# Kernel tuning notes

Hardware: AMD Instinct MI355X
Metric: run time of the kernel (lower is better)

Reference implementation:

```python
import jax, jax.numpy as jnp
import numpy as np

B, T, I, H, C = 128, 1024, 256, 512, 10


def setup_inputs() -> dict:
    key = jax.random.key(0)
    ks = jax.random.split(key, 11)
    s1 = 1.0 / np.sqrt(H)
    u = lambda k, shp, s: jax.random.uniform(k, shp, jnp.float32, -s, s)
    return {
        "x": jax.random.normal(ks[0], (B, T, I), jnp.float32),
        "w_ih1": u(ks[1], (H, I), s1),
        "w_hh1": u(ks[2], (H, H), s1),
        "b_ih1": u(ks[3], (H,), s1),
        "b_hh1": u(ks[4], (H,), s1),
        "w_ih2": u(ks[5], (H, H), s1),
        "w_hh2": u(ks[6], (H, H), s1),
        "b_ih2": u(ks[7], (H,), s1),
        "b_hh2": u(ks[8], (H,), s1),
        "w_out": u(ks[9], (C, H), s1),
        "b_out": u(ks[10], (C,), s1),
    }


def reference(x, w_ih1, w_hh1, b_ih1, b_hh1, w_ih2, w_hh2, b_ih2, b_hh2, w_out, b_out):
    batch = x.shape[0]
    h0 = jnp.zeros((batch, H), x.dtype)

    def step(carry, x_t):
        h1, h2 = carry
        # cell 1: tanh(x_t @ w_ih1^T + b_ih1 + h1 @ w_hh1^T + b_hh1)
        h1 = jnp.tanh(x_t @ w_ih1.T + b_ih1 + h1 @ w_hh1.T + b_hh1)
        # cell 2 takes h1 as input
        h2 = jnp.tanh(h1 @ w_ih2.T + b_ih2 + h2 @ w_hh2.T + b_hh2)
        return (h1, h2), None

    # scan over time: x transposed to [T, B, I]
    (h1_T, h2_T), _ = jax.lax.scan(step, (h0, h0), jnp.swapaxes(x, 0, 1))
    return h2_T @ w_out.T + b_out
```

## Files before the change

kernel.cpp:

```cpp
#include <hip/hip_runtime.h>
#include <hip/hip_fp16.h>

#define Tt 1024
#define Ii 256
#define Hh 512
#define Cc 10
#define SPINMAX (1 << 20)

typedef _Float16 f16;
typedef _Float16 f16x8 __attribute__((ext_vector_type(8)));
typedef _Float16 f16x4 __attribute__((ext_vector_type(4)));
typedef _Float16 f16x2 __attribute__((ext_vector_type(2)));
typedef float    f32x4 __attribute__((ext_vector_type(4)));

#define OFF_WH1   32768u
#define OFF_WH2   557056u
#define OFF_XWR   1081344u
#define OFF_H1R   3178496u
#define OFF_PAR   5275648u

#define FLG(i) (FL + (size_t)(i) * 32)

static __device__ __forceinline__ f32x4 mfma16(f16x8 a, f16x8 b, f32x4 c) {
  return __builtin_amdgcn_mfma_f32_16x16x32_f16(a, b, c, 0, 0, 0);
}
static __device__ __forceinline__ float fast_tanh(float v) {
  float e = __expf(2.0f * v);
  return 1.0f - 2.0f / (e + 1.0f);
}
static __device__ __forceinline__ int ldflag(const int* p) {
  return __hip_atomic_load(p, __ATOMIC_RELAXED, __HIP_MEMORY_SCOPE_AGENT);
}
static __device__ __forceinline__ void stflag(int* p, int v) {
  __hip_atomic_store(p, v, __ATOMIC_RELAXED, __HIP_MEMORY_SCOPE_AGENT);
}
static __device__ __forceinline__ f16x4 ld64cc(const f16* p) {
  union { unsigned long long u; f16x4 v; } U;
  U.u = __hip_atomic_load((const unsigned long long*)p, __ATOMIC_RELAXED, __HIP_MEMORY_SCOPE_AGENT);
  return U.v;
}
static __device__ __forceinline__ void st64cc(f16* p, f16x4 v) {
  union { unsigned long long u; f16x4 v; } U; U.v = v;
  __hip_atomic_store((unsigned long long*)p, U.u, __ATOMIC_RELAXED, __HIP_MEMORY_SCOPE_AGENT);
}
static __device__ __forceinline__ f16x8 ld128cc(const f16* p) {
  union { unsigned long long u[2]; f16x8 v; } U;
  U.u[0] = __hip_atomic_load((const unsigned long long*)p,     __ATOMIC_RELAXED, __HIP_MEMORY_SCOPE_AGENT);
  U.u[1] = __hip_atomic_load((const unsigned long long*)p + 1, __ATOMIC_RELAXED, __HIP_MEMORY_SCOPE_AGENT);
  return U.v;
}
static __device__ __forceinline__ void stu32cc(unsigned* p, unsigned v) {
  __hip_atomic_store(p, v, __ATOMIC_RELAXED, __HIP_MEMORY_SCOPE_AGENT);
}
static __device__ __forceinline__ int imin(int a, int b) { return a < b ? a : b; }

#define VMFENCE() asm volatile("s_waitcnt vmcnt(0)" ::: "memory")
#define LBAR() do { asm volatile("s_waitcnt lgkmcnt(0)" ::: "memory"); \
                    __builtin_amdgcn_s_barrier(); \
                    __builtin_amdgcn_sched_barrier(0); } while (0)

__global__ void prep_weights(const float* __restrict__ w_hh1,
                             const float* __restrict__ w_hh2,
                             char* __restrict__ ws) {
  f16* wh1 = (f16*)(ws + OFF_WH1);
  f16* wh2 = (f16*)(ws + OFF_WH2);
  int i = blockIdx.x * 512 + threadIdx.x;
  if (i < 512 * 512) { wh1[i] = (f16)w_hh1[i]; wh2[i] = (f16)w_hh2[i]; }
}

#define BODY(P, FVC, HAVC)                                                        \
  if (!dead) {                                                                    \
    const int p_ = (P);                                                           \
    const int s0_ = p_ & 3;                                                       \
                \
    if (isH1 && p_ >= 16) {                                                       \
      int g_ = imin(imin(rGa, rGb), imin(rGc, rGd));                              \
      if (g_ < p_ - 15) {                                                         \
        const int* g0 = FLG(80 + bg * 16 + s0_ * 4);                              \
        int v_ = 0, sp_ = 0;                                                      \
        do { v_ = imin(imin(ldflag(g0), ldflag(g0 + 32)),                         \
                       imin(ldflag(g0 + 64), ldflag(g0 + 96)));                   \
             if (v_ >= p_ - 15) break; __builtin_amdgcn_s_sleep(2);               \
        } while (++sp_ < SPINMAX);                                                \
        if (v_ < p_ - 15) dead = 1;                                               \
      }                                                                           \
    }                                                                             \
                                            \
    if (!(HAVC) && !dead) {                                                       \
      int v_ = 0, sp_ = 0;                                                        \
      if (isH1) {                                                                 \
        const int* f0 = FLG(16 + bg * 8 + s0_ * 2);                               \
        do { v_ = imin(ldflag(f0), ldflag(f0 + 32)); if (v_ >= p_ + 1) break;     \
             __builtin_amdgcn_s_sleep(2); } while (++sp_ < SPINMAX);              \
      } else {                                                                    \
        const int* f0 = FLG(80 + bg * 16 + s0_ * 4);                              \
        do { v_ = imin(imin(ldflag(f0), ldflag(f0 + 32)),                         \
                       imin(ldflag(f0 + 64), ldflag(f0 + 96)));                   \
             if (v_ >= p_ + 1) break; __builtin_amdgcn_s_sleep(2);                \
        } while (++sp_ < SPINMAX);                                                \
      }                                                                           \
      if (v_ < p_ + 1) dead = 1;                                                  \
      const f16* fs_ = fring + ((size_t)(p_ & 15) * 8 + bg) * 8192;               \
      FVC[0] = ld64cc(fs_ + (wid * 4 + 0) * 256 + lm * 16 + lgrp * 4);            \
      FVC[1] = ld64cc(fs_ + (wid * 4 + 1) * 256 + lm * 16 + lgrp * 4);            \
      FVC[2] = ld64cc(fs_ + (wid * 4 + 2) * 256 + lm * 16 + lgrp * 4);            \
      FVC[3] = ld64cc(fs_ + (wid * 4 + 3) * 256 + lm * 16 + lgrp * 4);            \
    }                                                                             \
      \
    f16x8 w15_[4];                                                                \
    if (p_ > 0) {                                                                 \
      _Pragma("unroll")                                                           \
      for (int nt = 0; nt < 4; ++nt)                                              \
        w15_[nt] = *(const f16x8*)&whh[(size_t)(wcol0 + nt * 16 + lm) * 512 + 15 * 32 + lk8]; \
    }                                                                             \
    f32x4 acc[4];                                                                 \
    acc[0] = f32x4{0.f, 0.f, 0.f, 0.f};                                           \
    acc[1] = acc[0]; acc[2] = acc[0]; acc[3] = acc[0];                            \
    if (p_ > 0) {                                                                 \
      _Pragma("unroll")                                                           \
      for (int kc = 0; kc < 16; ++kc) {                                           \
        f16x8 A_ = *(const f16x8*)&sH[lm * 520 + kc * 32 + lk8];                  \
        _Pragma("unroll")                                                         \
        for (int nt = 0; nt < 4; ++nt) {                                          \
          f16x8 B_;                                                               \
          if (kc < 4)       B_ = *(const f16x8*)&sB[((size_t)(kc * 4 + lgrp) * 512 + wcol0 + nt * 16 + lm) * 8]; \
          else if (kc < 15) B_ = wbr[kc - 4][nt];                                 \
          else              B_ = w15_[nt];                                        \
          acc[nt] = mfma16(A_, B_, acc[nt]);                                      \
        }                                                                         \
      }                                                                           \
    }                                                                             \
    LBAR();                                                 \
        \
    if (p_ > 0) {                                                                 \
      if (isH1) {                                                                 \
        if ((p_ & 3) == 0) { VMFENCE(); if (tid == 0) stflag(progF, p_); }        \
      } else {                                                                    \
        if ((p_ & 1) == 0 && tid == 0) stflag(progF, p_);                         \
      }                                                                           \
    }                                                                             \
                                                                    \
    _Pragma("unroll")                                                             \
    for (int nt = 0; nt < 4; ++nt) {                                              \
      acc[nt][0] += (float)FVC[nt][0]; acc[nt][1] += (float)FVC[nt][1];           \
      acc[nt][2] += (float)FVC[nt][2]; acc[nt][3] += (float)FVC[nt][3];           \
    }                                                                             \
                   \
    HAVC = 0;                                                                     \
    if (p_ + 2 < Tt && !dead) {                                                   \
      int ca_ = isH1 ? imin(rFa, rFb) : imin(imin(rFa, rFb), imin(rFc, rFd));     \
      if (ca_ >= p_ + 3) {                                                        \
        const f16* fs_ = fring + ((size_t)((p_ + 2) & 15) * 8 + bg) * 8192;       \
        FVC[0] = ld64cc(fs_ + (wid * 4 + 0) * 256 + lm * 16 + lgrp * 4);          \
        FVC[1] = ld64cc(fs_ + (wid * 4 + 1) * 256 + lm * 16 + lgrp * 4);          \
        FVC[2] = ld64cc(fs_ + (wid * 4 + 2) * 256 + lm * 16 + lgrp * 4);          \
        FVC[3] = ld64cc(fs_ + (wid * 4 + 3) * 256 + lm * 16 + lgrp * 4);          \
        HAVC = 1;                                                                 \
      }                                                                           \
    }                                                                             \
                              \
    unsigned* ring32_ = (unsigned*)(h1r + ((size_t)(p_ & 15) * 8 + bg) * 8192);   \
    _Pragma("unroll")                                                             \
    for (int nt = 0; nt < 4; ++nt) {                                              \
      const int cp_ = (wcol0 + nt * 16 + lm) >> 1;                                \
      float v0_ = fast_tanh(acc[nt][0]), v1_ = fast_tanh(acc[nt][1]);             \
      float v2_ = fast_tanh(acc[nt][2]), v3_ = fast_tanh(acc[nt][3]);             \
      float o0_ = __shfl_xor(v0_, 1, 64), o1_ = __shfl_xor(v1_, 1, 64);           \
      float o2_ = __shfl_xor(v2_, 1, 64), o3_ = __shfl_xor(v3_, 1, 64);           \
      float m_[4] = {v0_, v1_, v2_, v3_}, q_[4] = {o0_, o1_, o2_, o3_};           \
      _Pragma("unroll")                                                           \
      for (int r2 = 0; r2 < 2; ++r2) {                                            \
        const int rr_ = rlo + r2, row_ = lgrp * 4 + rr_;                          \
        float ve_ = (lane & 1) ? q_[rr_] : m_[rr_];                               \
        float vo_ = (lane & 1) ? m_[rr_] : q_[rr_];                               \
        union { f16x2 h; unsigned u; } P_; P_.h = f16x2{(f16)ve_, (f16)vo_};      \
        sH32[row_ * 260 + cp_] = P_.u;                                            \
        if (isH1) stu32cc(ring32_ + row_ * 256 + cp_, P_.u);                      \
      }                                                                           \
    }                                                                             \
                  \
    if (isH1) {                                                                   \
      const int* f0 = FLG(16 + bg * 8 + (((p_ + 3) & 3)) * 2);                    \
      rFa = ldflag(f0); rFb = ldflag(f0 + 32);                                    \
      const int* g0 = FLG(80 + bg * 16 + (((p_ + 1) & 3)) * 4);                   \
      rGa = ldflag(g0); rGb = ldflag(g0 + 32);                                    \
      rGc = ldflag(g0 + 64); rGd = ldflag(g0 + 96);                               \
    } else {                                                                      \
      const int* f0 = FLG(80 + bg * 16 + (((p_ + 3) & 3)) * 4);                   \
      rFa = ldflag(f0); rFb = ldflag(f0 + 32);                                    \
      rFc = ldflag(f0 + 64); rFd = ldflag(f0 + 96);                               \
    }                                                                             \
    LBAR();                                             \
  }

__global__ __launch_bounds__(512) __attribute__((amdgpu_waves_per_eu(2, 2)))
void rnn_main(
    const float* __restrict__ x,
    const float* __restrict__ w_ih1, const float* __restrict__ w_ih2,
    const float* __restrict__ b_ih1, const float* __restrict__ b_hh1,
    const float* __restrict__ b_ih2, const float* __restrict__ b_hh2,
    const float* __restrict__ w_out, const float* __restrict__ b_out,
    float* __restrict__ out, char* __restrict__ ws)
{
  __shared__ __align__(16) char LS[147712];

  int* FL = (int*)ws;
  const f16* wh1f = (const f16*)(ws + OFF_WH1);
  const f16* wh2f = (const f16*)(ws + OFF_WH2);
  f16* xwr  = (f16*)(ws + OFF_XWR);
  f16* h1r  = (f16*)(ws + OFF_H1R);
  f16* parr = (f16*)(ws + OFF_PAR);

  const int bid  = blockIdx.x;
  const int tid  = threadIdx.x;
  const int wid  = tid >> 6;
  const int lane = tid & 63;
  const int lm   = lane & 15;
  const int lgrp = lane >> 4;
  const int lk8  = lgrp * 8;
  const int rlo  = (lane & 1) * 2;

  if (bid < 16) {
    const bool isH1 = (bid < 8);
    const int bg = bid & 7;
    f16* sB = (f16*)LS;
    f16* sH = (f16*)(LS + 131072);
    unsigned* sH32 = (unsigned*)sH;
    const f16* whh = isH1 ? wh1f : wh2f;
    const f16* fring = isH1 ? xwr : parr;
    int* progF = FLG(isH1 ? bg : 8 + bg);
    const int wcol0 = wid * 64;

    for (int i = tid; i < 8192; i += 512) {
      const int kc = i >> 11, grp = (i >> 9) & 3, col = i & 511;
      *(f16x8*)&sB[(size_t)i * 8] =
        *(const f16x8*)&whh[(size_t)col * 512 + kc * 32 + grp * 8];
    }
    for (int i = tid; i < 16 * 260; i += 512) sH32[i] = 0u;
    f16x8 wbr[11][4];
    #pragma unroll
    for (int kr = 0; kr < 11; ++kr) {
      #pragma unroll
      for (int nt = 0; nt < 4; ++nt) {
        wbr[kr][nt] = *(const f16x8*)&whh[(size_t)(wcol0 + nt * 16 + lm) * 512 + (kr + 4) * 32 + lk8];
        asm volatile("" : "+v"(wbr[kr][nt]));
      }
    }
    __syncthreads();

    int dead = 0;
    f16x4 fX[4], fY[4];
    int hX = 0, hY = 0;
    int rFa = 0, rFb = 0, rFc = 0, rFd = 0;
    int rGa = 0, rGb = 0, rGc = 0, rGd = 0;

    {
      int v = 0, sp = 0;
      if (isH1) {
        const int* f0 = FLG(16 + bg * 8 + 0);
        do { v = imin(ldflag(f0), ldflag(f0 + 32)); if (v >= 1) break;
             __builtin_amdgcn_s_sleep(8); } while (++sp < SPINMAX);
      } else {
        const int* f0 = FLG(80 + bg * 16 + 0);
        do { v = imin(imin(ldflag(f0), ldflag(f0 + 32)),
                      imin(ldflag(f0 + 64), ldflag(f0 + 96)));
             if (v >= 1) break; __builtin_amdgcn_s_sleep(8); } while (++sp < SPINMAX);
      }
      if (v < 1) dead = 1;
      const f16* fs = fring + (size_t)bg * 8192;
      #pragma unroll
      for (int nt = 0; nt < 4; ++nt)
        fX[nt] = ld64cc(fs + (wid * 4 + nt) * 256 + lm * 16 + lgrp * 4);
      hX = 1;
      v = 0; sp = 0;
      if (isH1) {
        const int* f0 = FLG(16 + bg * 8 + 1 * 2);
        do { v = imin(ldflag(f0), ldflag(f0 + 32)); if (v >= 2) break;
             __builtin_amdgcn_s_sleep(8); } while (++sp < SPINMAX);
      } else {
        const int* f0 = FLG(80 + bg * 16 + 1 * 4);
        do { v = imin(imin(ldflag(f0), ldflag(f0 + 32)),
                      imin(ldflag(f0 + 64), ldflag(f0 + 96)));
             if (v >= 2) break; __builtin_amdgcn_s_sleep(8); } while (++sp < SPINMAX);
      }
      if (v < 2) dead = 1;
      const f16* fs1 = fring + ((size_t)1 * 8 + bg) * 8192;
      #pragma unroll
      for (int nt = 0; nt < 4; ++nt)
        fY[nt] = ld64cc(fs1 + (wid * 4 + nt) * 256 + lm * 16 + lgrp * 4);
      hY = 1;
      if (isH1) {
        const int* a0 = FLG(16 + bg * 8 + 2 * 2);
        rFa = ldflag(a0); rFb = ldflag(a0 + 32);
      } else {
        const int* a0 = FLG(80 + bg * 16 + 2 * 4);
        rFa = ldflag(a0); rFb = ldflag(a0 + 32);
        rFc = ldflag(a0 + 64); rFd = ldflag(a0 + 96);
      }
    }

    for (int p2 = 0; p2 < Tt; p2 += 2) {
      BODY(p2,     fX, hX)
      BODY(p2 + 1, fY, hY)
    }

    VMFENCE();
    if (tid == 0) stflag(progF, Tt + 2);

    if (!isH1) {
      const int rl = wid * 2 + (lane >> 5);
      const int l32 = lane & 31;
      const f16* hr = &sH[rl * 520 + l32 * 16];
      f16x8 h0 = *(const f16x8*)hr;
      f16x8 h1v = *(const f16x8*)(hr + 8);
      float hf[16];
      #pragma unroll
      for (int j = 0; j < 8; ++j) { hf[j] = (float)h0[j]; hf[8 + j] = (float)h1v[j]; }
      #pragma unroll
      for (int c = 0; c < Cc; ++c) {
        const float* wr_ = w_out + (size_t)c * Hh + l32 * 16;
        float s = 0.f;
        #pragma unroll
        for (int j4 = 0; j4 < 4; ++j4) {
          float4 w4 = *(const float4*)(wr_ + j4 * 4);
          s += hf[j4*4]*w4.x + hf[j4*4+1]*w4.y + hf[j4*4+2]*w4.z + hf[j4*4+3]*w4.w;
        }
        #pragma unroll
        for (int off = 16; off >= 1; off >>= 1) s += __shfl_xor(s, off, 64);
        if (l32 == 0) out[(bg * 16 + rl) * Cc + c] = s + b_out[c];
      }
    }
  } else if (bid < 144) {
    const int idx = bid - 16;
    const int bg = idx >> 4, r16 = idx & 15;
    const int set = r16 >> 2, cb = r16 & 3;
    f16* sW = (f16*)LS;
    f16* sA = (f16*)(LS + 131072);

    for (int i = tid; i < 8192; i += 512) {
      const int kc = i >> 9, grp = (i >> 7) & 3, cl = i & 127;
      const float* sp = w_ih2 + (size_t)(cb * 128 + cl) * 512 + kc * 32 + grp * 8;
      float4 a = *(const float4*)sp, b = *(const float4*)(sp + 4);
      *(f16x8*)&sW[(size_t)i * 8] =
        f16x8{(f16)a.x,(f16)a.y,(f16)a.z,(f16)a.w,(f16)b.x,(f16)b.y,(f16)b.z,(f16)b.w};
    }
    const int gcol = cb * 128 + wid * 16 + lm;
    const float bias2v = b_ih2[gcol] + b_hh2[gcol];
    __syncthreads();

    int* myf = FLG(80 + bg * 16 + set * 4 + cb);
    const int* fH1 = FLG(bg);
    const int* fH2 = FLG(8 + bg);
    const int row_ = tid >> 5, c32 = tid & 31;
    int dead = 0;
    f16x8 R0, R1;
    {
      int v = 0, sp = 0;
      do { v = ldflag(fH1); if (v >= set + 1) break;
           __builtin_amdgcn_s_sleep(8); } while (++sp < SPINMAX);
      if (v < set + 1) dead = 1;
      const f16* hs = h1r + ((size_t)(set & 15) * 8 + bg) * 8192;
      R0 = ld128cc(hs + (size_t)tid * 16);
      R1 = ld128cc(hs + (size_t)tid * 16 + 8);
    }
    int rH1 = ldflag(fH1), rH2 = ldflag(fH2);

    for (int q = set; q < Tt && !dead; q += 4) {
      VMFENCE();
      *(f16x8*)&sA[row_ * 520 + c32 * 16]     = R0;
      *(f16x8*)&sA[row_ * 520 + c32 * 16 + 8] = R1;
      __syncthreads();
      f32x4 acc = {bias2v, bias2v, bias2v, bias2v};
      #pragma unroll
      for (int kc = 0; kc < 16; ++kc) {
        f16x8 A = *(const f16x8*)&sA[lm * 520 + kc * 32 + lk8];
        f16x8 B = *(const f16x8*)&sW[((size_t)(kc * 4 + lgrp) * 128 + wid * 16 + lm) * 8];
        acc = mfma16(A, B, acc);
      }
      st64cc(parr + ((size_t)(q & 15) * 8 + bg) * 8192 + (cb * 8 + wid) * 256 + lm * 16 + lgrp * 4,
             f16x4{(f16)acc[0], (f16)acc[1], (f16)acc[2], (f16)acc[3]});
      VMFENCE();
      if (tid == 0) stflag(myf, q + 1);
      const int nq = q + 4;
      if (nq < Tt) {
        int haveR = 0;
        if (rH1 >= nq + 1) {
          const f16* hs = h1r + ((size_t)(nq & 15) * 8 + bg) * 8192;
          R0 = ld128cc(hs + (size_t)tid * 16);
          R1 = ld128cc(hs + (size_t)tid * 16 + 8);
          haveR = 1;
        }
        if (nq >= 16 && rH2 < nq - 15) {
          int v = 0, sp = 0;
          do { v = ldflag(fH2); if (v >= nq - 15) break;
               __builtin_amdgcn_s_sleep(4); } while (++sp < SPINMAX);
          if (v < nq - 15) dead = 1;
        }
        if (!haveR && !dead) {
          int v = 0, sp = 0;
          do { v = ldflag(fH1); if (v >= nq + 1) break;
               __builtin_amdgcn_s_sleep(4); } while (++sp < SPINMAX);
          if (v < nq + 1) dead = 1;
          const f16* hs = h1r + ((size_t)(nq & 15) * 8 + bg) * 8192;
          R0 = ld128cc(hs + (size_t)tid * 16);
          R1 = ld128cc(hs + (size_t)tid * 16 + 8);
        }
      }
      rH1 = ldflag(fH1); rH2 = ldflag(fH2);
      __syncthreads();
    }
    VMFENCE();
    if (tid == 0) stflag(myf, Tt + 2);
  } else {
    const int idx = bid - 144;
    const int bg = idx >> 3, r8 = idx & 7;
    const int set = r8 >> 1, half = r8 & 1;
    f16* sW = (f16*)LS;

    for (int i = tid; i < 8192; i += 512) {
      const int kc = i >> 10, grp = (i >> 8) & 3, cl = i & 255;
      const float* sp = w_ih1 + (size_t)(half * 256 + cl) * 256 + kc * 32 + grp * 8;
      float4 a = *(const float4*)sp, b = *(const float4*)(sp + 4);
      *(f16x8*)&sW[(size_t)i * 8] =
        f16x8{(f16)a.x,(f16)a.y,(f16)a.z,(f16)a.w,(f16)b.x,(f16)b.y,(f16)b.z,(f16)b.w};
    }
    const int gc0 = half * 256 + wid * 32 + lm;
    const float b1v0 = b_ih1[gc0] + b_hh1[gc0];
    const float b1v1 = b_ih1[gc0 + 16] + b_hh1[gc0 + 16];
    __syncthreads();

    int* myf = FLG(16 + bg * 8 + set * 2 + half);
    const int* fH1 = FLG(bg);
    int rH1 = 0, dead = 0;
    for (int t = set; t < Tt && !dead; t += 4) {
      if (t >= 16 && rH1 < t - 15) {
        int v = 0, sp = 0;
        do { v = ldflag(fH1); if (v >= t - 15) break;
             __builtin_amdgcn_s_sleep(4); } while (++sp < SPINMAX);
        if (v < t - 15) dead = 1;
      }
      f32x4 acc0 = {b1v0, b1v0, b1v0, b1v0};
      f32x4 acc1 = {b1v1, b1v1, b1v1, b1v1};
      const float* xr = x + ((size_t)(bg * 16 + lm) * Tt + t) * Ii + lk8;
      #pragma unroll
      for (int kc = 0; kc < 8; ++kc) {
        float4 a = *(const float4*)(xr + kc * 32);
        float4 b = *(const float4*)(xr + kc * 32 + 4);
        f16x8 A{(f16)a.x,(f16)a.y,(f16)a.z,(f16)a.w,(f16)b.x,(f16)b.y,(f16)b.z,(f16)b.w};
        acc0 = mfma16(A, *(const f16x8*)&sW[((size_t)(kc*4+lgrp)*256 + wid*32 + lm)*8], acc0);
        acc1 = mfma16(A, *(const f16x8*)&sW[((size_t)(kc*4+lgrp)*256 + wid*32 + 16 + lm)*8], acc1);
      }
      f16* dst = xwr + ((size_t)(t & 15) * 8 + bg) * 8192;
      st64cc(dst + (half*16 + wid*2 + 0)*256 + lm*16 + lgrp*4,
             f16x4{(f16)acc0[0],(f16)acc0[1],(f16)acc0[2],(f16)acc0[3]});
      st64cc(dst + (half*16 + wid*2 + 1)*256 + lm*16 + lgrp*4,
             f16x4{(f16)acc1[0],(f16)acc1[1],(f16)acc1[2],(f16)acc1[3]});
      VMFENCE();
      if (tid == 0) stflag(myf, t + 1);
      rH1 = ldflag(fH1);
    }
    if (tid == 0) stflag(myf, Tt + 2);
  }
}

extern "C" void kernel_launch(void* const* d_in, const int* in_sizes, int n_in,
                              void* d_out, int out_size, void* d_ws, size_t ws_size,
                              hipStream_t stream) {
  (void)in_sizes; (void)n_in; (void)out_size; (void)ws_size;
  const float* x     = (const float*)d_in[0];
  const float* w_ih1 = (const float*)d_in[1];
  const float* w_hh1 = (const float*)d_in[2];
  const float* b_ih1 = (const float*)d_in[3];
  const float* b_hh1 = (const float*)d_in[4];
  const float* w_ih2 = (const float*)d_in[5];
  const float* w_hh2 = (const float*)d_in[6];
  const float* b_ih2 = (const float*)d_in[7];
  const float* b_hh2 = (const float*)d_in[8];
  const float* w_out = (const float*)d_in[9];
  const float* b_out = (const float*)d_in[10];
  float* out = (float*)d_out;
  char* ws = (char*)d_ws;

  hipMemsetAsync(ws, 0, 32768, stream);
  hipLaunchKernelGGL(prep_weights, dim3(512), dim3(512), 0, stream, w_hh1, w_hh2, ws);
  hipLaunchKernelGGL(rnn_main, dim3(208), dim3(512), 0, stream,
                     x, w_ih1, w_ih2, b_ih1, b_hh1, b_ih2, b_hh2,
                     w_out, b_out, out, ws);
}
```

Measured before the change: 8.190 ms.

## Halve block size to 256 threads, doubling per-wave output tiles

Every role of the persistent RNN kernel now runs with 4 waves per block instead of 8. Each wave computes twice as many 16-column MFMA tiles, holding more weight fragments in registers (a 10x8 register-resident block plus two streamed k-chunks). The aim is to cut block-wide barrier cost on the serial recurrence and reuse each A fragment across more MFMAs. The cost is much higher register pressure and fewer waves to hide latency, so spilling or exposed memory latency is possible.

```diff
diff --git a/kernel.cpp b/kernel.cpp
--- a/kernel.cpp
+++ b/kernel.cpp
@@ -68,11 +68,18 @@
   if (i < 512 * 512) { wh1[i] = (f16)w_hh1[i]; wh2[i] = (f16)w_hh2[i]; }
 }
 
+#define FEEDLOAD(DST, SLOT) {                                                     \
+    const f16* fs_ = fring + ((size_t)(SLOT) * 8 + bg) * 8192;                    \
+    _Pragma("unroll")                                                             \
+    for (int nt = 0; nt < 8; ++nt)                                                \
+      DST[nt] = ld64cc(fs_ + (wid * 8 + nt) * 256 + lm * 16 + lgrp * 4);          \
+  }
+
 #define BODY(P, FVC, HAVC)                                                        \
   if (!dead) {                                                                    \
     const int p_ = (P);                                                           \
     const int s0_ = p_ & 3;                                                       \
-                \
+               \
     if (isH1 && p_ >= 16) {                                                       \
       int g_ = imin(imin(rGa, rGb), imin(rGc, rGd));                              \
       if (g_ < p_ - 15) {                                                         \
@@ -100,38 +107,36 @@
         } while (++sp_ < SPINMAX);                                                \
       }                                                                           \
       if (v_ < p_ + 1) dead = 1;                                                  \
-      const f16* fs_ = fring + ((size_t)(p_ & 15) * 8 + bg) * 8192;               \
-      FVC[0] = ld64cc(fs_ + (wid * 4 + 0) * 256 + lm * 16 + lgrp * 4);            \
-      FVC[1] = ld64cc(fs_ + (wid * 4 + 1) * 256 + lm * 16 + lgrp * 4);            \
-      FVC[2] = ld64cc(fs_ + (wid * 4 + 2) * 256 + lm * 16 + lgrp * 4);            \
-      FVC[3] = ld64cc(fs_ + (wid * 4 + 3) * 256 + lm * 16 + lgrp * 4);            \
-    }                                                                             \
-      \
-    f16x8 w15_[4];                                                                \
+      FEEDLOAD(FVC, p_ & 15)                                                      \
+    }                                                                             \
+          \
+    f16x8 w14_[8], w15_[8];                                                       \
     if (p_ > 0) {                                                                 \
       _Pragma("unroll")                                                           \
-      for (int nt = 0; nt < 4; ++nt)                                              \
+      for (int nt = 0; nt < 8; ++nt) {                                            \
+        w14_[nt] = *(const f16x8*)&whh[(size_t)(wcol0 + nt * 16 + lm) * 512 + 14 * 32 + lk8]; \
         w15_[nt] = *(const f16x8*)&whh[(size_t)(wcol0 + nt * 16 + lm) * 512 + 15 * 32 + lk8]; \
-    }                                                                             \
-    f32x4 acc[4];                                                                 \
-    acc[0] = f32x4{0.f, 0.f, 0.f, 0.f};                                           \
-    acc[1] = acc[0]; acc[2] = acc[0]; acc[3] = acc[0];                            \
+      }                                                                           \
+    }                                                                             \
+    f32x4 acc[8];                                                                 \
+    _Pragma("unroll")                                                             \
+    for (int nt = 0; nt < 8; ++nt) acc[nt] = f32x4{0.f, 0.f, 0.f, 0.f};           \
     if (p_ > 0) {                                                                 \
       _Pragma("unroll")                                                           \
       for (int kc = 0; kc < 16; ++kc) {                                           \
         f16x8 A_ = *(const f16x8*)&sH[lm * 520 + kc * 32 + lk8];                  \
         _Pragma("unroll")                                                         \
-        for (int nt = 0; nt < 4; ++nt) {                                          \
+        for (int nt = 0; nt < 8; ++nt) {                                          \
           f16x8 B_;                                                               \
           if (kc < 4)       B_ = *(const f16x8*)&sB[((size_t)(kc * 4 + lgrp) * 512 + wcol0 + nt * 16 + lm) * 8]; \
-          else if (kc < 15) B_ = wbr[kc - 4][nt];                                 \
+          else if (kc < 14) B_ = wbr[kc - 4][nt];                                 \
+          else if (kc == 14) B_ = w14_[nt];                                       \
           else              B_ = w15_[nt];                                        \
           acc[nt] = mfma16(A_, B_, acc[nt]);                                      \
         }                                                                         \
       }                                                                           \
     }                                                                             \
-    LBAR();                                                 \
-        \
+    LBAR();                            \
     if (p_ > 0) {                                                                 \
       if (isH1) {                                                                 \
         if ((p_ & 3) == 0) { VMFENCE(); if (tid == 0) stflag(progF, p_); }        \
@@ -139,29 +144,21 @@
         if ((p_ & 1) == 0 && tid == 0) stflag(progF, p_);                         \
       }                                                                           \
     }                                                                             \
-                                                                    \
     _Pragma("unroll")                                                             \
-    for (int nt = 0; nt < 4; ++nt) {                                              \
+    for (int nt = 0; nt < 8; ++nt) {                                              \
       acc[nt][0] += (float)FVC[nt][0]; acc[nt][1] += (float)FVC[nt][1];           \
       acc[nt][2] += (float)FVC[nt][2]; acc[nt][3] += (float)FVC[nt][3];           \
     }                                                                             \
-                   \
+              \
     HAVC = 0;                                                                     \
     if (p_ + 2 < Tt && !dead) {                                                   \
       int ca_ = isH1 ? imin(rFa, rFb) : imin(imin(rFa, rFb), imin(rFc, rFd));     \
-      if (ca_ >= p_ + 3) {                                                        \
-        const f16* fs_ = fring + ((size_t)((p_ + 2) & 15) * 8 + bg) * 8192;       \
-        FVC[0] = ld64cc(fs_ + (wid * 4 + 0) * 256 + lm * 16 + lgrp * 4);          \
-        FVC[1] = ld64cc(fs_ + (wid * 4 + 1) * 256 + lm * 16 + lgrp * 4);          \
-        FVC[2] = ld64cc(fs_ + (wid * 4 + 2) * 256 + lm * 16 + lgrp * 4);          \
-        FVC[3] = ld64cc(fs_ + (wid * 4 + 3) * 256 + lm * 16 + lgrp * 4);          \
-        HAVC = 1;                                                                 \
-      }                                                                           \
+      if (ca_ >= p_ + 3) { FEEDLOAD(FVC, (p_ + 2) & 15) HAVC = 1; }               \
     }                                                                             \
                               \
     unsigned* ring32_ = (unsigned*)(h1r + ((size_t)(p_ & 15) * 8 + bg) * 8192);   \
     _Pragma("unroll")                                                             \
-    for (int nt = 0; nt < 4; ++nt) {                                              \
+    for (int nt = 0; nt < 8; ++nt) {                                              \
       const int cp_ = (wcol0 + nt * 16 + lm) >> 1;                                \
       float v0_ = fast_tanh(acc[nt][0]), v1_ = fast_tanh(acc[nt][1]);             \
       float v2_ = fast_tanh(acc[nt][2]), v3_ = fast_tanh(acc[nt][3]);             \
@@ -178,7 +175,7 @@
         if (isH1) stu32cc(ring32_ + row_ * 256 + cp_, P_.u);                      \
       }                                                                           \
     }                                                                             \
-                  \
+             \
     if (isH1) {                                                                   \
       const int* f0 = FLG(16 + bg * 8 + (((p_ + 3) & 3)) * 2);                    \
       rFa = ldflag(f0); rFb = ldflag(f0 + 32);                                    \
@@ -193,7 +190,7 @@
     LBAR();                                             \
   }
 
-__global__ __launch_bounds__(512) __attribute__((amdgpu_waves_per_eu(2, 2)))
+__global__ __launch_bounds__(256) __attribute__((amdgpu_waves_per_eu(1)))
 void rnn_main(
     const float* __restrict__ x,
     const float* __restrict__ w_ih1, const float* __restrict__ w_ih2,
@@ -229,19 +226,19 @@
     const f16* whh = isH1 ? wh1f : wh2f;
     const f16* fring = isH1 ? xwr : parr;
     int* progF = FLG(isH1 ? bg : 8 + bg);
-    const int wcol0 = wid * 64;
-
-    for (int i = tid; i < 8192; i += 512) {
+    const int wcol0 = wid * 128;
+
+    for (int i = tid; i < 8192; i += 256) {
       const int kc = i >> 11, grp = (i >> 9) & 3, col = i & 511;
       *(f16x8*)&sB[(size_t)i * 8] =
         *(const f16x8*)&whh[(size_t)col * 512 + kc * 32 + grp * 8];
     }
-    for (int i = tid; i < 16 * 260; i += 512) sH32[i] = 0u;
-    f16x8 wbr[11][4];
+    for (int i = tid; i < 16 * 260; i += 256) sH32[i] = 0u;
+    f16x8 wbr[10][8];
     #pragma unroll
-    for (int kr = 0; kr < 11; ++kr) {
-      #pragma unroll
-      for (int nt = 0; nt < 4; ++nt) {
+    for (int kr = 0; kr < 10; ++kr) {
+      #pragma unroll
+      for (int nt = 0; nt < 8; ++nt) {
         wbr[kr][nt] = *(const f16x8*)&whh[(size_t)(wcol0 + nt * 16 + lm) * 512 + (kr + 4) * 32 + lk8];
         asm volatile("" : "+v"(wbr[kr][nt]));
       }
@@ -249,7 +246,7 @@
     __syncthreads();
 
     int dead = 0;
-    f16x4 fX[4], fY[4];
+    f16x4 fX[8], fY[8];
     int hX = 0, hY = 0;
     int rFa = 0, rFb = 0, rFc = 0, rFd = 0;
     int rGa = 0, rGb = 0, rGc = 0, rGd = 0;
@@ -267,10 +264,7 @@
              if (v >= 1) break; __builtin_amdgcn_s_sleep(8); } while (++sp < SPINMAX);
       }
       if (v < 1) dead = 1;
-      const f16* fs = fring + (size_t)bg * 8192;
-      #pragma unroll
-      for (int nt = 0; nt < 4; ++nt)
-        fX[nt] = ld64cc(fs + (wid * 4 + nt) * 256 + lm * 16 + lgrp * 4);
+      FEEDLOAD(fX, 0)
       hX = 1;
       v = 0; sp = 0;
       if (isH1) {
@@ -284,10 +278,7 @@
              if (v >= 2) break; __builtin_amdgcn_s_sleep(8); } while (++sp < SPINMAX);
       }
       if (v < 2) dead = 1;
-      const f16* fs1 = fring + ((size_t)1 * 8 + bg) * 8192;
-      #pragma unroll
-      for (int nt = 0; nt < 4; ++nt)
-        fY[nt] = ld64cc(fs1 + (wid * 4 + nt) * 256 + lm * 16 + lgrp * 4);
+      FEEDLOAD(fY, 1)
       hY = 1;
       if (isH1) {
         const int* a0 = FLG(16 + bg * 8 + 2 * 2);
@@ -308,26 +299,31 @@
     if (tid == 0) stflag(progF, Tt + 2);
 
     if (!isH1) {
-      const int rl = wid * 2 + (lane >> 5);
-      const int l32 = lane & 31;
-      const f16* hr = &sH[rl * 520 + l32 * 16];
-      f16x8 h0 = *(const f16x8*)hr;
-      f16x8 h1v = *(const f16x8*)(hr + 8);
-      float hf[16];
-      #pragma unroll
-      for (int j = 0; j < 8; ++j) { hf[j] = (float)h0[j]; hf[8 + j] = (float)h1v[j]; }
+      const int rl  = wid * 4 + (lane >> 4);
+      const int l16 = lane & 15;
+      const f16* hr = &sH[rl * 520 + l16 * 32];
+      f16x8 a0 = *(const f16x8*)hr;
+      f16x8 a1 = *(const f16x8*)(hr + 8);
+      f16x8 a2 = *(const f16x8*)(hr + 16);
+      f16x8 a3 = *(const f16x8*)(hr + 24);
+      float hf[32];
+      #pragma unroll
+      for (int j = 0; j < 8; ++j) {
+        hf[j] = (float)a0[j]; hf[8 + j] = (float)a1[j];
+        hf[16 + j] = (float)a2[j]; hf[24 + j] = (float)a3[j];
+      }
       #pragma unroll
       for (int c = 0; c < Cc; ++c) {
-        const float* wr_ = w_out + (size_t)c * Hh + l32 * 16;
+        const float* wr_ = w_out + (size_t)c * Hh + l16 * 32;
         float s = 0.f;
         #pragma unroll
-        for (int j4 = 0; j4 < 4; ++j4) {
+        for (int j4 = 0; j4 < 8; ++j4) {
           float4 w4 = *(const float4*)(wr_ + j4 * 4);
           s += hf[j4*4]*w4.x + hf[j4*4+1]*w4.y + hf[j4*4+2]*w4.z + hf[j4*4+3]*w4.w;
         }
         #pragma unroll
-        for (int off = 16; off >= 1; off >>= 1) s += __shfl_xor(s, off, 64);
-        if (l32 == 0) out[(bg * 16 + rl) * Cc + c] = s + b_out[c];
+        for (int off = 8; off >= 1; off >>= 1) s += __shfl_xor(s, off, 64);
+        if (l16 == 0) out[(bg * 16 + rl) * Cc + c] = s + b_out[c];
       }
     }
   } else if (bid < 144) {
@@ -337,57 +333,63 @@
     f16* sW = (f16*)LS;
     f16* sA = (f16*)(LS + 131072);
 
-    for (int i = tid; i < 8192; i += 512) {
+    for (int i = tid; i < 8192; i += 256) {
       const int kc = i >> 9, grp = (i >> 7) & 3, cl = i & 127;
       const float* sp = w_ih2 + (size_t)(cb * 128 + cl) * 512 + kc * 32 + grp * 8;
       float4 a = *(const float4*)sp, b = *(const float4*)(sp + 4);
       *(f16x8*)&sW[(size_t)i * 8] =
         f16x8{(f16)a.x,(f16)a.y,(f16)a.z,(f16)a.w,(f16)b.x,(f16)b.y,(f16)b.z,(f16)b.w};
     }
-    const int gcol = cb * 128 + wid * 16 + lm;
-    const float bias2v = b_ih2[gcol] + b_hh2[gcol];
+    const int gcol = cb * 128 + wid * 32 + lm;
+    const float b2v0 = b_ih2[gcol] + b_hh2[gcol];
+    const float b2v1 = b_ih2[gcol + 16] + b_hh2[gcol + 16];
     __syncthreads();
 
     int* myf = FLG(80 + bg * 16 + set * 4 + cb);
     const int* fH1 = FLG(bg);
     const int* fH2 = FLG(8 + bg);
-    const int row_ = tid >> 5, c32 = tid & 31;
+    const int srow = tid >> 4;
+    const int soff = (tid & 15) * 32;
     int dead = 0;
-    f16x8 R0, R1;
+    f16x8 R0, R1, R2, R3;
     {
       int v = 0, sp = 0;
       do { v = ldflag(fH1); if (v >= set + 1) break;
            __builtin_amdgcn_s_sleep(8); } while (++sp < SPINMAX);
       if (v < set + 1) dead = 1;
-      const f16* hs = h1r + ((size_t)(set & 15) * 8 + bg) * 8192;
-      R0 = ld128cc(hs + (size_t)tid * 16);
-      R1 = ld128cc(hs + (size_t)tid * 16 + 8);
+      const f16* hs = h1r + ((size_t)(set & 15) * 8 + bg) * 8192 + (size_t)tid * 32;
+      R0 = ld128cc(hs); R1 = ld128cc(hs + 8); R2 = ld128cc(hs + 16); R3 = ld128cc(hs + 24);
     }
     int rH1 = ldflag(fH1), rH2 = ldflag(fH2);
 
     for (int q = set; q < Tt && !dead; q += 4) {
       VMFENCE();
-      *(f16x8*)&sA[row_ * 520 + c32 * 16]     = R0;
-      *(f16x8*)&sA[row_ * 520 + c32 * 16 + 8] = R1;
+      *(f16x8*)&sA[srow * 520 + soff]      = R0;
+      *(f16x8*)&sA[srow * 520 + soff + 8]  = R1;
+      *(f16x8*)&sA[srow * 520 + soff + 16] = R2;
+      *(f16x8*)&sA[srow * 520 + soff + 24] = R3;
       __syncthreads();
-      f32x4 acc = {bias2v, bias2v, bias2v, bias2v};
+      f32x4 acc0 = {b2v0, b2v0, b2v0, b2v0};
+      f32x4 acc1 = {b2v1, b2v1, b2v1, b2v1};
       #pragma unroll
       for (int kc = 0; kc < 16; ++kc) {
         f16x8 A = *(const f16x8*)&sA[lm * 520 + kc * 32 + lk8];
-        f16x8 B = *(const f16x8*)&sW[((size_t)(kc * 4 + lgrp) * 128 + wid * 16 + lm) * 8];
-        acc = mfma16(A, B, acc);
-      }
-      st64cc(parr + ((size_t)(q & 15) * 8 + bg) * 8192 + (cb * 8 + wid) * 256 + lm * 16 + lgrp * 4,
-             f16x4{(f16)acc[0], (f16)acc[1], (f16)acc[2], (f16)acc[3]});
+        acc0 = mfma16(A, *(const f16x8*)&sW[((size_t)(kc * 4 + lgrp) * 128 + wid * 32 + lm) * 8], acc0);
+        acc1 = mfma16(A, *(const f16x8*)&sW[((size_t)(kc * 4 + lgrp) * 128 + wid * 32 + 16 + lm) * 8], acc1);
+      }
+      f16* dst = parr + ((size_t)(q & 15) * 8 + bg) * 8192;
+      st64cc(dst + (cb * 8 + wid * 2 + 0) * 256 + lm * 16 + lgrp * 4,
+             f16x4{(f16)acc0[0], (f16)acc0[1], (f16)acc0[2], (f16)acc0[3]});
+      st64cc(dst + (cb * 8 + wid * 2 + 1) * 256 + lm * 16 + lgrp * 4,
+             f16x4{(f16)acc1[0], (f16)acc1[1], (f16)acc1[2], (f16)acc1[3]});
       VMFENCE();
       if (tid == 0) stflag(myf, q + 1);
       const int nq = q + 4;
       if (nq < Tt) {
         int haveR = 0;
         if (rH1 >= nq + 1) {
-          const f16* hs = h1r + ((size_t)(nq & 15) * 8 + bg) * 8192;
-          R0 = ld128cc(hs + (size_t)tid * 16);
-          R1 = ld128cc(hs + (size_t)tid * 16 + 8);
+          const f16* hs = h1r + ((size_t)(nq & 15) * 8 + bg) * 8192 + (size_t)tid * 32;
+          R0 = ld128cc(hs); R1 = ld128cc(hs + 8); R2 = ld128cc(hs + 16); R3 = ld128cc(hs + 24);
           haveR = 1;
         }
         if (nq >= 16 && rH2 < nq - 15) {
@@ -401,9 +403,8 @@
           do { v = ldflag(fH1); if (v >= nq + 1) break;
                __builtin_amdgcn_s_sleep(4); } while (++sp < SPINMAX);
           if (v < nq + 1) dead = 1;
-          const f16* hs = h1r + ((size_t)(nq & 15) * 8 + bg) * 8192;
-          R0 = ld128cc(hs + (size_t)tid * 16);
-          R1 = ld128cc(hs + (size_t)tid * 16 + 8);
+          const f16* hs = h1r + ((size_t)(nq & 15) * 8 + bg) * 8192 + (size_t)tid * 32;
+          R0 = ld128cc(hs); R1 = ld128cc(hs + 8); R2 = ld128cc(hs + 16); R3 = ld128cc(hs + 24);
         }
       }
       rH1 = ldflag(fH1); rH2 = ldflag(fH2);
@@ -417,16 +418,18 @@
     const int set = r8 >> 1, half = r8 & 1;
     f16* sW = (f16*)LS;
 
-    for (int i = tid; i < 8192; i += 512) {
+    for (int i = tid; i < 8192; i += 256) {
       const int kc = i >> 10, grp = (i >> 8) & 3, cl = i & 255;
       const float* sp = w_ih1 + (size_t)(half * 256 + cl) * 256 + kc * 32 + grp * 8;
       float4 a = *(const float4*)sp, b = *(const float4*)(sp + 4);
       *(f16x8*)&sW[(size_t)i * 8] =
         f16x8{(f16)a.x,(f16)a.y,(f16)a.z,(f16)a.w,(f16)b.x,(f16)b.y,(f16)b.z,(f16)b.w};
     }
-    const int gc0 = half * 256 + wid * 32 + lm;
-    const float b1v0 = b_ih1[gc0] + b_hh1[gc0];
-    const float b1v1 = b_ih1[gc0 + 16] + b_hh1[gc0 + 16];
+    const int gc0 = half * 256 + wid * 64 + lm;
+    float b1v[4];
+    #pragma unroll
+    for (int nt = 0; nt < 4; ++nt)
+      b1v[nt] = b_ih1[gc0 + nt * 16] + b_hh1[gc0 + nt * 16];
     __syncthreads();
 
     int* myf = FLG(16 + bg * 8 + set * 2 + half);
@@ -439,22 +442,24 @@
              __builtin_amdgcn_s_sleep(4); } while (++sp < SPINMAX);
         if (v < t - 15) dead = 1;
       }
-      f32x4 acc0 = {b1v0, b1v0, b1v0, b1v0};
-      f32x4 acc1 = {b1v1, b1v1, b1v1, b1v1};
+      f32x4 acc[4];
+      #pragma unroll
+      for (int nt = 0; nt < 4; ++nt) acc[nt] = f32x4{b1v[nt], b1v[nt], b1v[nt], b1v[nt]};
       const float* xr = x + ((size_t)(bg * 16 + lm) * Tt + t) * Ii + lk8;
       #pragma unroll
       for (int kc = 0; kc < 8; ++kc) {
         float4 a = *(const float4*)(xr + kc * 32);
         float4 b = *(const float4*)(xr + kc * 32 + 4);
         f16x8 A{(f16)a.x,(f16)a.y,(f16)a.z,(f16)a.w,(f16)b.x,(f16)b.y,(f16)b.z,(f16)b.w};
-        acc0 = mfma16(A, *(const f16x8*)&sW[((size_t)(kc*4+lgrp)*256 + wid*32 + lm)*8], acc0);
-        acc1 = mfma16(A, *(const f16x8*)&sW[((size_t)(kc*4+lgrp)*256 + wid*32 + 16 + lm)*8], acc1);
+        #pragma unroll
+        for (int nt = 0; nt < 4; ++nt)
+          acc[nt] = mfma16(A, *(const f16x8*)&sW[((size_t)(kc*4+lgrp)*256 + wid*64 + nt*16 + lm)*8], acc[nt]);
       }
       f16* dst = xwr + ((size_t)(t & 15) * 8 + bg) * 8192;
-      st64cc(dst + (half*16 + wid*2 + 0)*256 + lm*16 + lgrp*4,
-             f16x4{(f16)acc0[0],(f16)acc0[1],(f16)acc0[2],(f16)acc0[3]});
-      st64cc(dst + (half*16 + wid*2 + 1)*256 + lm*16 + lgrp*4,
-             f16x4{(f16)acc1[0],(f16)acc1[1],(f16)acc1[2],(f16)acc1[3]});
+      #pragma unroll
+      for (int nt = 0; nt < 4; ++nt)
+        st64cc(dst + (half * 16 + wid * 4 + nt) * 256 + lm * 16 + lgrp * 4,
+               f16x4{(f16)acc[nt][0], (f16)acc[nt][1], (f16)acc[nt][2], (f16)acc[nt][3]});
       VMFENCE();
       if (tid == 0) stflag(myf, t + 1);
       rH1 = ldflag(fH1);
@@ -483,7 +488,7 @@
 
   hipMemsetAsync(ws, 0, 32768, stream);
   hipLaunchKernelGGL(prep_weights, dim3(512), dim3(512), 0, stream, w_hh1, w_hh2, ws);
-  hipLaunchKernelGGL(rnn_main, dim3(208), dim3(512), 0, stream,
+  hipLaunchKernelGGL(rnn_main, dim3(208), dim3(256), 0, stream,
                      x, w_ih1, w_ih2, b_ih1, b_hh1, b_ih2, b_hh2,
                      w_out, b_out, out, ws);
 }
```

Measured after the change: 13.58 ms. 65.8% more time.
